# Kernel optimization log

Measured on AMD Instinct MI355X. Metric: run time of the kernel, lower is better.

Reference implementation:

```python
import jax, jax.numpy as jnp
import numpy as np

FT = 0.2  # clip floor (init arg ft)

def _norm_mat(m):
    # matrix / (count of nonzeros along last dim + 1e-30)
    deg = jnp.sum(m != 0, axis=-1, keepdims=True).astype(m.dtype)
    return m / (deg + 1e-30)

def _l2n(x):
    return x / (jnp.linalg.norm(x, axis=-1, keepdims=True) + 1e-30)

def setup_inputs():
    B, L, D, H, O = 2, 2048, 64, 64, 128
    N = 2 * L
    ks = jax.random.split(jax.random.key(0), 30)
    u = lambda i, s: jax.random.uniform(ks[i], s, jnp.float32)
    g = lambda i, s: jax.random.normal(ks[i], s, jnp.float32) * 0.05
    inp = {}
    inp['word_outputs_0'] = g(0, (B, L, D))
    inp['word_outputs_1'] = g(1, (B, L, D))
    inp['node_hidden'] = g(2, (B, D))
    inp['op_embedding'] = g(3, (B, O, D))
    inp['word_exist_sequence'] = (u(4, (B, N)) < 0.8).astype(jnp.float32)
    inp['word_exist_matrix'] = (u(5, (B, N, N)) < 0.8).astype(jnp.float32)
    inp['word_operator'] = (u(6, (B, N, O)) < 0.02).astype(jnp.float32)
    inp['word_word'] = (u(7, (B, N, N)) < 0.01).astype(jnp.float32)
    inp['depend_0'] = (u(8, (B, L, L)) < 0.05).astype(jnp.float32)
    inp['depend_1'] = (u(9, (B, L, L)) < 0.05).astype(jnp.float32)
    inp['goal_word'] = u(10, (B, N))
    names = [('Wg', (D, H)), ('bg', (H,)), ('Wwk', (D, H)), ('bwk', (H,)),
             ('Wws', (D, H)), ('bws', (H,)), ('Wo', (D, D)), ('bo', (D,)),
             ('Wupd', (3 * H, D)), ('bupd', (D,)), ('Wf', (3 * H + D, D)), ('bf', (D,)),
             ('Wf2', (2 * D, D)), ('bf2', (D,)), ('Wout', (D, D)), ('bout', (D,))]
    for i, (nm, s) in enumerate(names):
        inp[nm] = g(11 + i, s)
    return inp

def _forward(w0, w1, nh, opE, wes, wem, wop, ww, d0, d1, gw,
             Wg, bg, Wwk, bwk, Wws, bws, Wo, bo, Wupd, bupd, Wf, bf, Wf2, bf2, Wout, bout):
    all_w = jnp.concatenate([w0, w1], axis=1)                      # [B,N,D]
    goal_trans = (nh @ Wg + bg)[:, None, :]                        # [B,1,H] (broadcast = expand)
    word_g = _l2n(goal_trans * gw[..., None])                      # [B,N,H]
    word_w_k = _l2n(jnp.matmul(_norm_mat(ww * wem), all_w @ Wwk + bwk))
    ws0 = jnp.matmul(_norm_mat(d0), w0 @ Wws + bws)
    ws1 = jnp.matmul(_norm_mat(d1), w1 @ Wws + bws)
    word_w_s = _l2n(jnp.concatenate([ws0, ws1], axis=1))           # [B,N,H]
    neigh = jnp.concatenate([word_g, word_w_k, word_w_s], axis=-1)  # [B,N,3H]
    forget = jax.nn.sigmoid(jnp.concatenate([all_w, word_g, word_w_k, word_w_s], axis=-1) @ Wf + bf)
    word_updated = jnp.maximum(forget, FT) * all_w + (1.0 - forget) * jax.nn.relu(neigh @ Wupd + bupd)
    adj_op = _norm_mat(jnp.swapaxes(wes[..., None] * wop, 1, 2))   # [B,O,N]
    word_op = jnp.matmul(adj_op, word_updated @ Wo + bo)           # [B,O,D]
    forget2 = jax.nn.sigmoid(jnp.concatenate([opE, word_op], axis=-1) @ Wf2 + bf2)
    op_out = jnp.maximum(forget2, FT) * opE + (1.0 - forget2) * jax.nn.relu(word_op @ Wout + bout)
    # original returns (split(word_updated), op_embedding); concat along node axis here
    return jnp.concatenate([word_updated, op_out], axis=1)         # [B,N+O,D]

def reference(word_outputs_0, word_outputs_1, node_hidden, op_embedding,
              word_exist_sequence, word_exist_matrix, word_operator, word_word,
              depend_0, depend_1, goal_word,
              Wg, bg, Wwk, bwk, Wws, bws, Wo, bo, Wupd, bupd, Wf, bf, Wf2, bf2, Wout, bout):
    return _forward(word_outputs_0, word_outputs_1, node_hidden, op_embedding,
                    word_exist_sequence, word_exist_matrix, word_operator, word_word,
                    depend_0, depend_1, goal_word,
                    Wg, bg, Wwk, bwk, Wws, bws, Wo, bo, Wupd, bupd, Wf, bf, Wf2, bf2, Wout, bout)
```

## Files before the change

kernel.cpp:

```cpp
#include <hip/hip_runtime.h>
#include <cstdint>

typedef unsigned short u16;
typedef unsigned long long u64;

__device__ __forceinline__ u16 f2b(float f){
  union { float f; uint32_t i; } v; v.f = f;
  uint32_t r = v.i + 0x7FFFu + ((v.i >> 16) & 1u);
  return (u16)(r >> 16);
}
__device__ __forceinline__ float b2f(u16 u){
  union { uint32_t i; float f; } v; v.i = ((uint32_t)u) << 16; return v.f;
}
__device__ __forceinline__ float sigmoidf(float x){ return 1.0f / (1.0f + __expf(-x)); }

__global__ __launch_bounds__(256) void k_prep(
    const float* __restrict__ w0, const float* __restrict__ w1,
    uint32_t* __restrict__ wpk){
  int tid = threadIdx.x, blk = blockIdx.x;
  int b = blk >> 6;
  int j = (blk & 63) * 64 + (tid >> 2);
  int part = tid & 3;
  const float* src = (j < 2048) ? (w0 + ((size_t)(b*2048 + j))*64 + part*16)
                                : (w1 + ((size_t)(b*2048 + j - 2048))*64 + part*16);
  uint32_t* dst = wpk + ((size_t)b*4096 + j)*32 + part*8;
  float4 v0 = ((const float4*)src)[0];
  float4 v1 = ((const float4*)src)[1];
  float4 v2 = ((const float4*)src)[2];
  float4 v3 = ((const float4*)src)[3];
  uint4 o0, o1;
  o0.x = (uint32_t)f2b(v0.x) | ((uint32_t)f2b(v0.y) << 16);
  o0.y = (uint32_t)f2b(v0.z) | ((uint32_t)f2b(v0.w) << 16);
  o0.z = (uint32_t)f2b(v1.x) | ((uint32_t)f2b(v1.y) << 16);
  o0.w = (uint32_t)f2b(v1.z) | ((uint32_t)f2b(v1.w) << 16);
  o1.x = (uint32_t)f2b(v2.x) | ((uint32_t)f2b(v2.y) << 16);
  o1.y = (uint32_t)f2b(v2.z) | ((uint32_t)f2b(v2.w) << 16);
  o1.z = (uint32_t)f2b(v3.x) | ((uint32_t)f2b(v3.y) << 16);
  o1.w = (uint32_t)f2b(v3.z) | ((uint32_t)f2b(v3.w) << 16);
  ((uint4*)dst)[0] = o0;
  ((uint4*)dst)[1] = o1;
}

__global__ __launch_bounds__(256) void k_bits(
    const float* __restrict__ ww, const float* __restrict__ wem,
    const float* __restrict__ d0, const float* __restrict__ d1,
    const float* __restrict__ wes, const float* __restrict__ wop,
    const uint32_t* __restrict__ wpk,
    const float* __restrict__ nh, const float* __restrict__ Wg, const float* __restrict__ bg,
    const float* __restrict__ Wf, const float* __restrict__ Wupd, const float* __restrict__ Wo,
    u16* __restrict__ psumB, int* __restrict__ pcntB,
    u16* __restrict__ psumD, int* __restrict__ pcntD,
    u64* __restrict__ bitOp, float* __restrict__ ghat,
    uint32_t* __restrict__ pkWf, uint32_t* __restrict__ pkWu, uint32_t* __restrict__ pkWo){
  __shared__ int q[4][288];
  int tid = threadIdx.x, wave = tid >> 6, lane = tid & 63;
  int bid = blockIdx.x;
  if (bid >= 2048){
    if (bid >= 2304){
      int aux = bid - 2304;
      if (aux == 16){
        if (tid < 128){
          int b = tid >> 6, h = tid & 63;
          float g = bg[h];
          for (int d = 0; d < 64; ++d) g += nh[b*64 + d] * Wg[d*64 + h];
          float ss = g * g;
          #pragma unroll
          for (int o = 32; o > 0; o >>= 1) ss += __shfl_xor(ss, o, 64);
          ghat[b*64 + h] = g / (sqrtf(ss) + 1e-30f);
        }
        return;
      }
      for (int k = tid; k < 1024; k += 256){
        int i = aux*1024 + k;
        const float* src; uint32_t* dst; int li;
        if (i < 8192){ src = Wf; dst = pkWf; li = i; }
        else if (i < 14336){ src = Wupd; dst = pkWu; li = i - 8192; }
        else { src = Wo; dst = pkWo; li = i - 14336; }
        int k2 = li >> 6, ln = li & 63;
        dst[li] = (uint32_t)f2b(src[(2*k2)*64 + ln]) | ((uint32_t)f2b(src[(2*k2+1)*64 + ln]) << 16);
      }
      return;
    }
    int w = (bid - 2048)*4 + wave;
    int ng0 = w * 8;
    #pragma unroll
    for (int i = 0; i < 8; ++i){
      int n = ng0 + i;
      float vx = wop[(size_t)n*128 + lane];
      float vy = wop[(size_t)n*128 + 64 + lane];
      float e  = wes[n];
      u64 m0 = __ballot((e != 0.f) && (vx != 0.f));
      u64 m1 = __ballot((e != 0.f) && (vy != 0.f));
      if (lane == 0) bitOp[(size_t)n*2]     = m0;
      if (lane == 1) bitOp[(size_t)n*2 + 1] = m1;
    }
    return;
  }
  int wid = bid*4 + wave;
  int half = lane >> 5, dcol = lane & 31;
  int colhi = (lane >> 2) * 256 + (lane & 3);
  float4 a[8];
  u64 myw = 0;
  const float4* r0 = (const float4*)(ww + (size_t)wid*4096) + lane;
  #pragma unroll
  for (int i = 0; i < 8; ++i) a[i] = r0[i*64];
#define BAL8(wb) { \
  _Pragma("unroll") for (int i = 0; i < 8; ++i){ \
    u64 m0 = __ballot(a[i].x != 0.f); \
    u64 m1 = __ballot(a[i].y != 0.f); \
    u64 m2 = __ballot(a[i].z != 0.f); \
    u64 m3 = __ballot(a[i].w != 0.f); \
    if (lane == (wb) + i*4 + 0) myw = m0; \
    if (lane == (wb) + i*4 + 1) myw = m1; \
    if (lane == (wb) + i*4 + 2) myw = m2; \
    if (lane == (wb) + i*4 + 3) myw = m3; } }
  BAL8(0)
  #pragma unroll
  for (int i = 0; i < 8; ++i) a[i] = r0[512 + i*64];
  BAL8(32)
  int c = __popcll(myw);
  int pre = c;
  #pragma unroll
  for (int off = 1; off < 64; off <<= 1){
    int tt = __shfl_up(pre, off, 64);
    if (lane >= off) pre += tt;
  }
  int total = __shfl(pre, 63, 64);
  int base = pre - c;
  u64 m = myw;
  while (m){
    int p = __builtin_ctzll(m); m &= m - 1;
    q[wave][base++] = colhi + p*4;
  }
  int totP = (total + 31) & ~31;
  if (lane < totP - total) q[wave][total + lane] = 0;
  const float* depBase; int jadd, bdep;
  if (wid < 4096){ depBase = d0 + (size_t)wid*2048; jadd = 0; bdep = wid >> 11; }
  else { int rr = wid - 4096; depBase = d1 + (size_t)rr*2048; jadd = 2048; bdep = rr >> 11; }
  {
    const float4* r2 = (const float4*)depBase + lane;
    #pragma unroll
    for (int i = 0; i < 8; ++i) a[i] = r2[i*64];
  }
  {
    int b = wid >> 12;
    const uint32_t* wub = wpk + (size_t)b*131072 + dcol;
    const float* wemRow = wem + (size_t)wid*4096;
    float accE = 0.f, accO = 0.f, vcF = 0.f;
    int nb = totP >> 5;
    uint32_t g0[16], g1[16];
    float m0a[16], m1a[16];
#define GISSB(arr, wma, bi) { int bse = (bi) << 5; \
  _Pragma("unroll") for (int k2 = 0; k2 < 16; ++k2){ \
    int j = q[wave][bse + 2*k2 + half]; \
    arr[k2] = wub[(size_t)j*32]; \
    wma[k2] = wemRow[j]; } }
#define GACCB(arr, wma, bi) { int bse = (bi) << 5; \
  _Pragma("unroll") for (int k2 = 0; k2 < 16; ++k2){ \
    float sel = ((bse + 2*k2 + half) < total) ? wma[k2] : 0.f; \
    uint32_t wv = arr[k2]; \
    accE += sel * b2f((u16)wv); \
    accO += sel * b2f((u16)(wv >> 16)); \
    vcF += sel; } }
    if (nb > 0) GISSB(g0, m0a, 0)
    for (int bi = 0; bi < nb; bi += 2){
      if (bi + 1 < nb) GISSB(g1, m1a, bi + 1)
      GACCB(g0, m0a, bi)
      if (bi + 1 < nb){
        if (bi + 2 < nb) GISSB(g0, m0a, bi + 2)
        GACCB(g1, m1a, bi + 1)
      }
    }
#undef GISSB
#undef GACCB
    accE += __shfl_xor(accE, 32, 64);
    accO += __shfl_xor(accO, 32, 64);
    vcF  += __shfl_xor(vcF, 32, 64);
    if (lane < 32)
      ((uint32_t*)(psumB + (size_t)wid*64))[lane] =
        (uint32_t)f2b(accE) | ((uint32_t)f2b(accO) << 16);
    if (lane == 0) pcntB[wid] = (int)(vcF + 0.5f);
  }
  myw = 0;
  BAL8(0)
#undef BAL8
  c = __popcll(myw);
  pre = c;
  #pragma unroll
  for (int off = 1; off < 64; off <<= 1){
    int tt = __shfl_up(pre, off, 64);
    if (lane >= off) pre += tt;
  }
  total = __shfl(pre, 63, 64);
  base = pre - c;
  m = myw;
  while (m){
    int p = __builtin_ctzll(m); m &= m - 1;
    q[wave][base++] = colhi + p*4;
  }
  totP = (total + 31) & ~31;
  if (lane < totP - total) q[wave][total + lane] = 0;
  {
    const uint32_t* wub = wpk + (size_t)bdep*131072 + (size_t)jadd*32 + dcol;
    float accE = 0.f, accO = 0.f;
    int nb = totP >> 5;
    uint32_t g0[16], g1[16];
#define GISS(arr, bi) { int bse = (bi) << 5; \
  _Pragma("unroll") for (int k2 = 0; k2 < 16; ++k2){ \
    int j = q[wave][bse + 2*k2 + half]; \
    arr[k2] = wub[(size_t)j*32]; } }
#define GACC(arr, bi) { int bse = (bi) << 5; \
  _Pragma("unroll") for (int k2 = 0; k2 < 16; ++k2){ \
    bool v = (bse + 2*k2 + half) < total; \
    uint32_t wv = arr[k2]; \
    accE += v ? b2f((u16)wv) : 0.f; \
    accO += v ? b2f((u16)(wv >> 16)) : 0.f; } }
    if (nb > 0) GISS(g0, 0)
    for (int bi = 0; bi < nb; bi += 2){
      if (bi + 1 < nb) GISS(g1, bi + 1)
      GACC(g0, bi)
      if (bi + 1 < nb){
        if (bi + 2 < nb) GISS(g0, bi + 2)
        GACC(g1, bi + 1)
      }
    }
#undef GISS
#undef GACC
    accE += __shfl_xor(accE, 32, 64);
    accO += __shfl_xor(accO, 32, 64);
    if (lane < 32)
      ((uint32_t*)(psumD + (size_t)wid*64))[lane] =
        (uint32_t)f2b(accE) | ((uint32_t)f2b(accO) << 16);
    if (lane == 0) pcntD[wid] = total;
  }
}

__global__ __launch_bounds__(256, 2) void k_mid(
    const u16* __restrict__ psumB, const int* __restrict__ pcntB,
    const u16* __restrict__ psumD, const int* __restrict__ pcntD,
    const float* __restrict__ Wwk, const float* __restrict__ bwk,
    const float* __restrict__ Wws, const float* __restrict__ bws,
    const float* __restrict__ w0, const float* __restrict__ w1,
    const float* __restrict__ gw, const float* __restrict__ ghat,
    const uint32_t* __restrict__ pkWf, const uint32_t* __restrict__ pkWu,
    const uint32_t* __restrict__ pkWo,
    const float* __restrict__ bf, const float* __restrict__ bupd, const float* __restrict__ bo,
    float* __restrict__ out, float* __restrict__ WUo){
  __shared__ uint32_t ldsU[16384];
  __shared__ float xsh[4][256];
  int tid = threadIdx.x, lane = tid & 63, wave = tid >> 6;
  float* sWk = (float*)ldsU;
  float* sWs = (float*)ldsU + 4096;
  for (int i = tid; i < 1024; i += 256){
    ((float4*)sWk)[i] = ((const float4*)Wwk)[i];
    ((float4*)sWs)[i] = ((const float4*)Wws)[i];
  }
  __syncthreads();
  float bwkL = bwk[lane], bwsL = bws[lane];
  float wk[4], wsv[4], aw[4], wgv[4];
  #pragma unroll
  for (int t = 0; t < 4; ++t){
    int row = blockIdx.x*4 + wave + t*2048;
    int b = row >> 12, n = row & 4095;
    float S = b2f(psumB[(size_t)row*64 + lane]);
    int T = pcntB[row];
    float y = (float)T * bwkL;
    #pragma unroll 8
    for (int d = 0; d < 64; ++d) y += __shfl(S, d, 64) * sWk[d*64 + lane];
    float ss = y * y;
    #pragma unroll
    for (int o = 32; o > 0; o >>= 1) ss += __shfl_xor(ss, o, 64);
    wk[t] = y / (sqrtf(ss) + 1e-30f);
    int rp = (n < 2048) ? (b*2048 + n) : (4096 + b*2048 + (n - 2048));
    float S2 = b2f(psumD[(size_t)rp*64 + lane]);
    int T2 = pcntD[rp];
    float y2 = (float)T2 * bwsL;
    #pragma unroll 8
    for (int d = 0; d < 64; ++d) y2 += __shfl(S2, d, 64) * sWs[d*64 + lane];
    float ss2 = y2 * y2;
    #pragma unroll
    for (int o = 32; o > 0; o >>= 1) ss2 += __shfl_xor(ss2, o, 64);
    wsv[t] = y2 / (sqrtf(ss2) + 1e-30f);
    aw[t] = (n < 2048) ? w0[((size_t)(b*2048 + n))*64 + lane]
                       : w1[((size_t)(b*2048 + n - 2048))*64 + lane];
    wgv[t] = (gw[b*4096 + n] != 0.f) ? ghat[b*64 + lane] : 0.f;
  }
  __syncthreads();
  uint32_t* pWf = ldsU;
  uint32_t* pWu = ldsU + 8192;
  uint32_t* pWo = ldsU + 14336;
  for (int i = tid; i < 2048; i += 256) ((uint4*)pWf)[i] = ((const uint4*)pkWf)[i];
  for (int i = tid; i < 1536; i += 256) ((uint4*)pWu)[i] = ((const uint4*)pkWu)[i];
  for (int i = tid; i < 512;  i += 256) ((uint4*)pWo)[i] = ((const uint4*)pkWo)[i];
  __syncthreads();
  float bff = bf[lane], bup = bupd[lane], boo = bo[lane];
  #pragma unroll
  for (int t = 0; t < 4; ++t){
    int row = blockIdx.x*4 + wave + t*2048;
    int b = row >> 12, n = row & 4095;
    xsh[wave][lane] = aw[t]; xsh[wave][64 + lane] = wgv[t];
    xsh[wave][128 + lane] = wk[t]; xsh[wave][192 + lane] = wsv[t];
    float f = bff, u = bup;
    #pragma unroll 8
    for (int k2 = 0; k2 < 32; ++k2){
      float2 xv = *(const float2*)&xsh[wave][2*k2];
      uint32_t wf = pWf[k2*64 + lane];
      f += xv.x * b2f((u16)wf) + xv.y * b2f((u16)(wf >> 16));
    }
    #pragma unroll 8
    for (int k2 = 32; k2 < 128; ++k2){
      float2 xv = *(const float2*)&xsh[wave][2*k2];
      uint32_t wf = pWf[k2*64 + lane];
      uint32_t wu = pWu[(k2 - 32)*64 + lane];
      f += xv.x * b2f((u16)wf) + xv.y * b2f((u16)(wf >> 16));
      u += xv.x * b2f((u16)wu) + xv.y * b2f((u16)(wu >> 16));
    }
    f = sigmoidf(f);
    u = fmaxf(u, 0.f);
    float wu = fmaxf(f, 0.2f) * aw[t] + (1.f - f) * u;
    out[((size_t)b*4224 + n)*64 + lane] = wu;
    float o = boo;
    #pragma unroll 8
    for (int k2 = 0; k2 < 32; ++k2){
      uint32_t wo2 = pWo[k2*64 + lane];
      o += __shfl(wu, 2*k2, 64) * b2f((u16)wo2) + __shfl(wu, 2*k2 + 1, 64) * b2f((u16)(wo2 >> 16));
    }
    WUo[(size_t)row*64 + lane] = o;
  }
}

__global__ __launch_bounds__(256) void k_opfin(
    const u64* __restrict__ bitOp, const float* __restrict__ WUo,
    const float* __restrict__ opE,
    const float* __restrict__ Wf2, const float* __restrict__ bf2,
    const float* __restrict__ Wout, const float* __restrict__ bout,
    float* __restrict__ out){
  __shared__ float sW2[8192];
  __shared__ float sWo[4096];
  __shared__ int q[4][96];
  __shared__ float sacc[4][64];
  __shared__ int scnt[4];
  __shared__ float xsh[128];
  int tid = threadIdx.x, lane = tid & 63, wave = tid >> 6;
  for (int i = tid; i < 2048; i += 256) ((float4*)sW2)[i] = ((const float4*)Wf2)[i];
  for (int i = tid; i < 1024; i += 256) ((float4*)sWo)[i] = ((const float4*)Wout)[i];
  int rowIdx = blockIdx.x;
  int b = rowIdx >> 7, o = rowIdx & 127;
  int wrd = o >> 6, bit = o & 63;
  const u64* bp = bitOp + (size_t)b*8192 + (size_t)wave*2048 + wrd;
  u64 lt = (1ULL << lane) - 1ULL;
  u64 vv[16];
  #pragma unroll
  for (int it = 0; it < 16; ++it) vv[it] = bp[(size_t)(it*64 + lane)*2];
  int cnt = 0;
  #pragma unroll
  for (int it = 0; it < 16; ++it){
    bool nz = (vv[it] >> bit) & 1ULL;
    u64 m = __ballot(nz);
    if (nz) q[wave][cnt + (int)__popcll(m & lt)] = wave*1024 + it*64 + lane;
    cnt += (int)__popcll(m);
  }
  const float* Xb = WUo + (size_t)b*4096*64 + lane;
  float acc = 0.f;
  int i = 0;
  for (; i + 8 <= cnt; i += 8){
    int4 c0 = *(const int4*)&q[wave][i];
    int4 c1 = *(const int4*)&q[wave][i + 4];
    float v0 = Xb[(size_t)c0.x*64], v1 = Xb[(size_t)c0.y*64];
    float v2 = Xb[(size_t)c0.z*64], v3 = Xb[(size_t)c0.w*64];
    float v4 = Xb[(size_t)c1.x*64], v5 = Xb[(size_t)c1.y*64];
    float v6 = Xb[(size_t)c1.z*64], v7 = Xb[(size_t)c1.w*64];
    acc += ((v0 + v1) + (v2 + v3)) + ((v4 + v5) + (v6 + v7));
  }
  for (; i < cnt; ++i) acc += Xb[(size_t)q[wave][i]*64];
  sacc[wave][lane] = acc;
  if (lane == 0) scnt[wave] = cnt;
  __syncthreads();
  if (wave == 0){
    float t = sacc[0][lane] + sacc[1][lane] + sacc[2][lane] + sacc[3][lane];
    float deg = (float)(scnt[0] + scnt[1] + scnt[2] + scnt[3]);
    float wo = t / (deg + 1e-30f);
    float e  = opE[(size_t)rowIdx*64 + lane];
    xsh[lane] = e; xsh[64 + lane] = wo;
    float f = bf2[lane], u = bout[lane];
    #pragma unroll 8
    for (int k = 0; k < 128; ++k) f += xsh[k] * sW2[k*64 + lane];
    #pragma unroll 8
    for (int d = 0; d < 64; ++d)  u += xsh[64 + d] * sWo[d*64 + lane];
    f = sigmoidf(f);
    u = fmaxf(u, 0.f);
    float res = fmaxf(f, 0.2f) * e + (1.f - f) * u;
    out[((size_t)b*4224 + 4096 + o)*64 + lane] = res;
  }
}

extern "C" void kernel_launch(void* const* d_in, const int* in_sizes, int n_in,
                              void* d_out, int out_size, void* d_ws, size_t ws_size,
                              hipStream_t stream){
  const float* w0   = (const float*)d_in[0];
  const float* w1   = (const float*)d_in[1];
  const float* nh   = (const float*)d_in[2];
  const float* opE  = (const float*)d_in[3];
  const float* wes  = (const float*)d_in[4];
  const float* wem  = (const float*)d_in[5];
  const float* wop  = (const float*)d_in[6];
  const float* ww   = (const float*)d_in[7];
  const float* d0   = (const float*)d_in[8];
  const float* d1   = (const float*)d_in[9];
  const float* gw   = (const float*)d_in[10];
  const float* Wg   = (const float*)d_in[11];
  const float* bg   = (const float*)d_in[12];
  const float* Wwk  = (const float*)d_in[13];
  const float* bwk  = (const float*)d_in[14];
  const float* Wws  = (const float*)d_in[15];
  const float* bws  = (const float*)d_in[16];
  const float* Wo   = (const float*)d_in[17];
  const float* bo   = (const float*)d_in[18];
  const float* Wupd = (const float*)d_in[19];
  const float* bupd = (const float*)d_in[20];
  const float* Wf   = (const float*)d_in[21];
  const float* bf   = (const float*)d_in[22];
  const float* Wf2  = (const float*)d_in[23];
  const float* bf2  = (const float*)d_in[24];
  const float* Wout = (const float*)d_in[25];
  const float* bout = (const float*)d_in[26];

  float* ws    = (float*)d_ws;
  float* ghat  = ws;
  uint32_t* pkWf = (uint32_t*)(ws + 128);
  uint32_t* pkWu = (uint32_t*)(ws + 8320);
  uint32_t* pkWo = (uint32_t*)(ws + 14464);
  u64*  bitOp  = (u64*)(ws + 16512);
  u16*  psumB  = (u16*)(ws + 49280);
  int*  pcntB  = (int*)(ws + 311424);
  u16*  psumD  = (u16*)(ws + 319616);
  int*  pcntD  = (int*)(ws + 581760);
  float* WUo   = ws + 589952;
  uint32_t* wpk = (uint32_t*)(ws + 1114240);
  float* out   = (float*)d_out;

  k_prep<<<128, 256, 0, stream>>>(w0, w1, wpk);
  k_bits<<<2321, 256, 0, stream>>>(ww, wem, d0, d1, wes, wop, wpk,
                                   nh, Wg, bg, Wf, Wupd, Wo,
                                   psumB, pcntB, psumD, pcntD,
                                   bitOp, ghat, pkWf, pkWu, pkWo);
  k_mid<<<512, 256, 0, stream>>>(psumB, pcntB, psumD, pcntD,
                                 Wwk, bwk, Wws, bws, w0, w1, gw, ghat,
                                 pkWf, pkWu, pkWo, bf, bupd, bo, out, WUo);
  k_opfin<<<256, 256, 0, stream>>>(bitOp, WUo, opE, Wf2, bf2, Wout, bout, out);
}
```

Baseline: 410.9 us.

## Split fused sparse-gather kernel into separate ww and dependency kernels

Splits the former k_bits kernel into k_big, which handles the word_word×exist_matrix row gather, and k_dep, which handles the dependency gather plus the auxiliary op-bitmask and weight-packing work. It also halves the gather batch from 32 to 16 indices per step, shrinking the register arrays and the padding rounding. The aim is lower register pressure and higher occupancy for each gather phase, and less wasted padded work on sparse rows. The cost is an extra kernel launch, and the dependency work no longer overlaps within the same wave as the ww work.

```diff
diff --git a/kernel.cpp b/kernel.cpp
--- a/kernel.cpp
+++ b/kernel.cpp
@@ -41,14 +41,99 @@
   ((uint4*)dst)[1] = o1;
 }
 
-__global__ __launch_bounds__(256) void k_bits(
+#define BAL8(wb) { \
+  _Pragma("unroll") for (int i = 0; i < 8; ++i){ \
+    u64 m0 = __ballot(a[i].x != 0.f); \
+    u64 m1 = __ballot(a[i].y != 0.f); \
+    u64 m2 = __ballot(a[i].z != 0.f); \
+    u64 m3 = __ballot(a[i].w != 0.f); \
+    if (lane == (wb) + i*4 + 0) myw = m0; \
+    if (lane == (wb) + i*4 + 1) myw = m1; \
+    if (lane == (wb) + i*4 + 2) myw = m2; \
+    if (lane == (wb) + i*4 + 3) myw = m3; } }
+
+#define COMPACT() \
+  int c = __popcll(myw); \
+  int pre = c; \
+  _Pragma("unroll") \
+  for (int off = 1; off < 64; off <<= 1){ \
+    int tt = __shfl_up(pre, off, 64); \
+    if (lane >= off) pre += tt; \
+  } \
+  int total = __shfl(pre, 63, 64); \
+  int base = pre - c; \
+  u64 m = myw; \
+  while (m){ \
+    int p = __builtin_ctzll(m); m &= m - 1; \
+    q[wave][base++] = colhi + p*4; \
+  } \
+  int totP = (total + 15) & ~15; \
+  if (lane < totP - total) q[wave][total + lane] = 0;
+
+__global__ __launch_bounds__(256) void k_big(
     const float* __restrict__ ww, const float* __restrict__ wem,
+    const uint32_t* __restrict__ wpk,
+    u16* __restrict__ psumB, int* __restrict__ pcntB){
+  __shared__ int q[4][288];
+  int tid = threadIdx.x, wave = tid >> 6, lane = tid & 63;
+  int wid = blockIdx.x*4 + wave;
+  int half = lane >> 5, dcol = lane & 31;
+  int colhi = (lane >> 2) * 256 + (lane & 3);
+  float4 a[8];
+  u64 myw = 0;
+  const float4* r0 = (const float4*)(ww + (size_t)wid*4096) + lane;
+  #pragma unroll
+  for (int i = 0; i < 8; ++i) a[i] = r0[i*64];
+  BAL8(0)
+  #pragma unroll
+  for (int i = 0; i < 8; ++i) a[i] = r0[512 + i*64];
+  BAL8(32)
+  COMPACT()
+  int b = wid >> 12;
+  const uint32_t* wub = wpk + (size_t)b*131072 + dcol;
+  const float* wemRow = wem + (size_t)wid*4096;
+  float accE = 0.f, accO = 0.f, vcF = 0.f;
+  int nb = totP >> 4;
+  uint32_t g0[8], g1[8];
+  float m0a[8], m1a[8];
+#define GISSB(arr, wma, bi) { int bse = (bi) << 4; \
+  _Pragma("unroll") for (int k2 = 0; k2 < 8; ++k2){ \
+    int j = q[wave][bse + 2*k2 + half]; \
+    arr[k2] = wub[(size_t)j*32]; \
+    wma[k2] = wemRow[j]; } }
+#define GACCB(arr, wma, bi) { int bse = (bi) << 4; \
+  _Pragma("unroll") for (int k2 = 0; k2 < 8; ++k2){ \
+    float sel = ((bse + 2*k2 + half) < total) ? wma[k2] : 0.f; \
+    uint32_t wv = arr[k2]; \
+    accE += sel * b2f((u16)wv); \
+    accO += sel * b2f((u16)(wv >> 16)); \
+    vcF += sel; } }
+  if (nb > 0) GISSB(g0, m0a, 0)
+  for (int bi = 0; bi < nb; bi += 2){
+    if (bi + 1 < nb) GISSB(g1, m1a, bi + 1)
+    GACCB(g0, m0a, bi)
+    if (bi + 1 < nb){
+      if (bi + 2 < nb) GISSB(g0, m0a, bi + 2)
+      GACCB(g1, m1a, bi + 1)
+    }
+  }
+#undef GISSB
+#undef GACCB
+  accE += __shfl_xor(accE, 32, 64);
+  accO += __shfl_xor(accO, 32, 64);
+  vcF  += __shfl_xor(vcF, 32, 64);
+  if (lane < 32)
+    ((uint32_t*)(psumB + (size_t)wid*64))[lane] =
+      (uint32_t)f2b(accE) | ((uint32_t)f2b(accO) << 16);
+  if (lane == 0) pcntB[wid] = (int)(vcF + 0.5f);
+}
+
+__global__ __launch_bounds__(256) void k_dep(
     const float* __restrict__ d0, const float* __restrict__ d1,
     const float* __restrict__ wes, const float* __restrict__ wop,
     const uint32_t* __restrict__ wpk,
     const float* __restrict__ nh, const float* __restrict__ Wg, const float* __restrict__ bg,
     const float* __restrict__ Wf, const float* __restrict__ Wupd, const float* __restrict__ Wo,
-    u16* __restrict__ psumB, int* __restrict__ pcntB,
     u16* __restrict__ psumD, int* __restrict__ pcntD,
     u64* __restrict__ bitOp, float* __restrict__ ghat,
     uint32_t* __restrict__ pkWf, uint32_t* __restrict__ pkWu, uint32_t* __restrict__ pkWo){
@@ -99,140 +184,49 @@
   int wid = bid*4 + wave;
   int half = lane >> 5, dcol = lane & 31;
   int colhi = (lane >> 2) * 256 + (lane & 3);
-  float4 a[8];
-  u64 myw = 0;
-  const float4* r0 = (const float4*)(ww + (size_t)wid*4096) + lane;
-  #pragma unroll
-  for (int i = 0; i < 8; ++i) a[i] = r0[i*64];
-#define BAL8(wb) { \
-  _Pragma("unroll") for (int i = 0; i < 8; ++i){ \
-    u64 m0 = __ballot(a[i].x != 0.f); \
-    u64 m1 = __ballot(a[i].y != 0.f); \
-    u64 m2 = __ballot(a[i].z != 0.f); \
-    u64 m3 = __ballot(a[i].w != 0.f); \
-    if (lane == (wb) + i*4 + 0) myw = m0; \
-    if (lane == (wb) + i*4 + 1) myw = m1; \
-    if (lane == (wb) + i*4 + 2) myw = m2; \
-    if (lane == (wb) + i*4 + 3) myw = m3; } }
-  BAL8(0)
-  #pragma unroll
-  for (int i = 0; i < 8; ++i) a[i] = r0[512 + i*64];
-  BAL8(32)
-  int c = __popcll(myw);
-  int pre = c;
-  #pragma unroll
-  for (int off = 1; off < 64; off <<= 1){
-    int tt = __shfl_up(pre, off, 64);
-    if (lane >= off) pre += tt;
-  }
-  int total = __shfl(pre, 63, 64);
-  int base = pre - c;
-  u64 m = myw;
-  while (m){
-    int p = __builtin_ctzll(m); m &= m - 1;
-    q[wave][base++] = colhi + p*4;
-  }
-  int totP = (total + 31) & ~31;
-  if (lane < totP - total) q[wave][total + lane] = 0;
   const float* depBase; int jadd, bdep;
   if (wid < 4096){ depBase = d0 + (size_t)wid*2048; jadd = 0; bdep = wid >> 11; }
   else { int rr = wid - 4096; depBase = d1 + (size_t)rr*2048; jadd = 2048; bdep = rr >> 11; }
+  float4 a[8];
+  u64 myw = 0;
   {
     const float4* r2 = (const float4*)depBase + lane;
     #pragma unroll
     for (int i = 0; i < 8; ++i) a[i] = r2[i*64];
   }
-  {
-    int b = wid >> 12;
-    const uint32_t* wub = wpk + (size_t)b*131072 + dcol;
-    const float* wemRow = wem + (size_t)wid*4096;
-    float accE = 0.f, accO = 0.f, vcF = 0.f;
-    int nb = totP >> 5;
-    uint32_t g0[16], g1[16];
-    float m0a[16], m1a[16];
-#define GISSB(arr, wma, bi) { int bse = (bi) << 5; \
-  _Pragma("unroll") for (int k2 = 0; k2 < 16; ++k2){ \
-    int j = q[wave][bse + 2*k2 + half]; \
-    arr[k2] = wub[(size_t)j*32]; \
-    wma[k2] = wemRow[j]; } }
-#define GACCB(arr, wma, bi) { int bse = (bi) << 5; \
-  _Pragma("unroll") for (int k2 = 0; k2 < 16; ++k2){ \
-    float sel = ((bse + 2*k2 + half) < total) ? wma[k2] : 0.f; \
-    uint32_t wv = arr[k2]; \
-    accE += sel * b2f((u16)wv); \
-    accO += sel * b2f((u16)(wv >> 16)); \
-    vcF += sel; } }
-    if (nb > 0) GISSB(g0, m0a, 0)
-    for (int bi = 0; bi < nb; bi += 2){
-      if (bi + 1 < nb) GISSB(g1, m1a, bi + 1)
-      GACCB(g0, m0a, bi)
-      if (bi + 1 < nb){
-        if (bi + 2 < nb) GISSB(g0, m0a, bi + 2)
-        GACCB(g1, m1a, bi + 1)
-      }
-    }
-#undef GISSB
-#undef GACCB
-    accE += __shfl_xor(accE, 32, 64);
-    accO += __shfl_xor(accO, 32, 64);
-    vcF  += __shfl_xor(vcF, 32, 64);
-    if (lane < 32)
-      ((uint32_t*)(psumB + (size_t)wid*64))[lane] =
-        (uint32_t)f2b(accE) | ((uint32_t)f2b(accO) << 16);
-    if (lane == 0) pcntB[wid] = (int)(vcF + 0.5f);
-  }
-  myw = 0;
   BAL8(0)
-#undef BAL8
-  c = __popcll(myw);
-  pre = c;
-  #pragma unroll
-  for (int off = 1; off < 64; off <<= 1){
-    int tt = __shfl_up(pre, off, 64);
-    if (lane >= off) pre += tt;
-  }
-  total = __shfl(pre, 63, 64);
-  base = pre - c;
-  m = myw;
-  while (m){
-    int p = __builtin_ctzll(m); m &= m - 1;
-    q[wave][base++] = colhi + p*4;
-  }
-  totP = (total + 31) & ~31;
-  if (lane < totP - total) q[wave][total + lane] = 0;
-  {
-    const uint32_t* wub = wpk + (size_t)bdep*131072 + (size_t)jadd*32 + dcol;
-    float accE = 0.f, accO = 0.f;
-    int nb = totP >> 5;
-    uint32_t g0[16], g1[16];
-#define GISS(arr, bi) { int bse = (bi) << 5; \
-  _Pragma("unroll") for (int k2 = 0; k2 < 16; ++k2){ \
+  COMPACT()
+  const uint32_t* wub = wpk + (size_t)bdep*131072 + (size_t)jadd*32 + dcol;
+  float accE = 0.f, accO = 0.f;
+  int nb = totP >> 4;
+  uint32_t g0[8], g1[8];
+#define GISS(arr, bi) { int bse = (bi) << 4; \
+  _Pragma("unroll") for (int k2 = 0; k2 < 8; ++k2){ \
     int j = q[wave][bse + 2*k2 + half]; \
     arr[k2] = wub[(size_t)j*32]; } }
-#define GACC(arr, bi) { int bse = (bi) << 5; \
-  _Pragma("unroll") for (int k2 = 0; k2 < 16; ++k2){ \
+#define GACC(arr, bi) { int bse = (bi) << 4; \
+  _Pragma("unroll") for (int k2 = 0; k2 < 8; ++k2){ \
     bool v = (bse + 2*k2 + half) < total; \
     uint32_t wv = arr[k2]; \
     accE += v ? b2f((u16)wv) : 0.f; \
     accO += v ? b2f((u16)(wv >> 16)) : 0.f; } }
-    if (nb > 0) GISS(g0, 0)
-    for (int bi = 0; bi < nb; bi += 2){
-      if (bi + 1 < nb) GISS(g1, bi + 1)
-      GACC(g0, bi)
-      if (bi + 1 < nb){
-        if (bi + 2 < nb) GISS(g0, bi + 2)
-        GACC(g1, bi + 1)
-      }
-    }
+  if (nb > 0) GISS(g0, 0)
+  for (int bi = 0; bi < nb; bi += 2){
+    if (bi + 1 < nb) GISS(g1, bi + 1)
+    GACC(g0, bi)
+    if (bi + 1 < nb){
+      if (bi + 2 < nb) GISS(g0, bi + 2)
+      GACC(g1, bi + 1)
+    }
+  }
 #undef GISS
 #undef GACC
-    accE += __shfl_xor(accE, 32, 64);
-    accO += __shfl_xor(accO, 32, 64);
-    if (lane < 32)
-      ((uint32_t*)(psumD + (size_t)wid*64))[lane] =
-        (uint32_t)f2b(accE) | ((uint32_t)f2b(accO) << 16);
-    if (lane == 0) pcntD[wid] = total;
-  }
+  accE += __shfl_xor(accE, 32, 64);
+  accO += __shfl_xor(accO, 32, 64);
+  if (lane < 32)
+    ((uint32_t*)(psumD + (size_t)wid*64))[lane] =
+      (uint32_t)f2b(accE) | ((uint32_t)f2b(accO) << 16);
+  if (lane == 0) pcntD[wid] = total;
 }
 
 __global__ __launch_bounds__(256, 2) void k_mid(
@@ -440,10 +434,10 @@
   float* out   = (float*)d_out;
 
   k_prep<<<128, 256, 0, stream>>>(w0, w1, wpk);
-  k_bits<<<2321, 256, 0, stream>>>(ww, wem, d0, d1, wes, wop, wpk,
-                                   nh, Wg, bg, Wf, Wupd, Wo,
-                                   psumB, pcntB, psumD, pcntD,
-                                   bitOp, ghat, pkWf, pkWu, pkWo);
+  k_big<<<2048, 256, 0, stream>>>(ww, wem, wpk, psumB, pcntB);
+  k_dep<<<2321, 256, 0, stream>>>(d0, d1, wes, wop, wpk,
+                                  nh, Wg, bg, Wf, Wupd, Wo,
+                                  psumD, pcntD, bitOp, ghat, pkWf, pkWu, pkWo);
   k_mid<<<512, 256, 0, stream>>>(psumB, pcntB, psumD, pcntD,
                                  Wwk, bwk, Wws, bws, w0, w1, gw, ghat,
                                  pkWf, pkWu, pkWo, bf, bupd, bo, out, WUo);
```

After: 414.1 us. No clear change (+0.8%).
